# Kernel optimization log

Measured on AMD Instinct MI355X. Metric: run time of the kernel, lower is better.

The kernel has to match this reference:

```python
import jax, jax.numpy as jnp
import numpy as np

NUM_HEADS = 16
DIM_MODEL = 1024
DIM_K = DIM_MODEL // NUM_HEADS
B, S = 2, 2048


def _linear_params(key, d_in, d_out):
    kw, kb = jax.random.split(key)
    bound = 1.0 / np.sqrt(d_in)
    W = jax.random.uniform(kw, (d_out, d_in), jnp.float32, -bound, bound)
    b = jax.random.uniform(kb, (d_out,), jnp.float32, -bound, bound)
    return W, b


def setup_inputs() -> dict:
    key = jax.random.key(0)
    ks = jax.random.split(key, 7)
    Q_in = jax.random.normal(ks[0], (B, S, DIM_MODEL), jnp.float32)
    K_in = jax.random.normal(ks[1], (B, S, DIM_MODEL), jnp.float32)
    V_in = jax.random.normal(ks[2], (B, S, DIM_MODEL), jnp.float32)
    Wq, bq = _linear_params(ks[3], DIM_MODEL, DIM_MODEL)
    Wk, bk = _linear_params(ks[4], DIM_MODEL, DIM_MODEL)
    Wv, bv = _linear_params(ks[5], DIM_MODEL, DIM_MODEL)
    Wo, bo = _linear_params(ks[6], DIM_MODEL, DIM_MODEL)
    return {"Q_in": Q_in, "K_in": K_in, "V_in": V_in,
            "Wq": Wq, "bq": bq, "Wk": Wk, "bk": bk,
            "Wv": Wv, "bv": bv, "Wo": Wo, "bo": bo}


def reference(Q_in, K_in, V_in, Wq, bq, Wk, bk, Wv, bv, Wo, bo):
    # QKV projections (nn.Linear: x @ W.T + b)
    Q = Q_in @ Wq.T + bq
    K = K_in @ Wk.T + bk
    V = V_in @ Wv.T + bv
    # [B, S, D] -> [B, H, S, dk]
    def split_heads(x):
        return x.reshape(B, S, NUM_HEADS, DIM_K).transpose(0, 2, 1, 3)
    Qh, Kh, Vh = split_heads(Q), split_heads(K), split_heads(V)
    # Scaled dot-product attention
    scale = 1.0 / np.sqrt(DIM_K)
    scores = jnp.einsum('bhqd,bhkd->bhqk', Qh, Kh) * scale  # [B,H,S,S]
    attn = jax.nn.softmax(scores, axis=-1)
    out = jnp.einsum('bhqk,bhkd->bhqd', attn, Vh)  # [B,H,S,dk]
    # Merge heads -> [B, S, D]
    out = out.transpose(0, 2, 1, 3).reshape(B, S, DIM_MODEL)
    return out @ Wo.T + bo
```

## Files before the change

### kernel.cpp

```cpp
#include <hip/hip_runtime.h>
#include <stdint.h>

#define BB 2
#define SS 2048
#define DD 1024
#define HH 16
#define DKK 64
#define MT (BB*SS)

#define GSTRIDE 40

#define QSCALE 0.18033688011112042f

using short8  = __attribute__((ext_vector_type(8))) short;
using floatx4 = __attribute__((ext_vector_type(4))) float;
using u16x4   = __attribute__((ext_vector_type(4))) unsigned short;
typedef unsigned short u16;

__device__ __forceinline__ float ex2(float x) { return __builtin_amdgcn_exp2f(x); }

__device__ __forceinline__ u16 f2b(float f) {
  union { float f; unsigned u; } v; v.f = f;
  return (u16)((v.u + 0x7FFFu + ((v.u >> 16) & 1u)) >> 16);
}
__device__ __forceinline__ unsigned cvt_pk_bf16(float lo, float hi) {
  unsigned r;
  asm("v_cvt_pk_bf16_f32 %0, %1, %2" : "=v"(r) : "v"(lo), "v"(hi));
  return r;
}
__device__ __forceinline__ void pack16(const float4* p, short8& lo, short8& hi) {
  float4 x0 = p[0], x1 = p[1], x2 = p[2], x3 = p[3];
  lo[0]=(short)f2b(x0.x); lo[1]=(short)f2b(x0.y); lo[2]=(short)f2b(x0.z); lo[3]=(short)f2b(x0.w);
  lo[4]=(short)f2b(x1.x); lo[5]=(short)f2b(x1.y); lo[6]=(short)f2b(x1.z); lo[7]=(short)f2b(x1.w);
  hi[0]=(short)f2b(x2.x); hi[1]=(short)f2b(x2.y); hi[2]=(short)f2b(x2.z); hi[3]=(short)f2b(x2.w);
  hi[4]=(short)f2b(x3.x); hi[5]=(short)f2b(x3.y); hi[6]=(short)f2b(x3.z); hi[7]=(short)f2b(x3.w);
}
__device__ __forceinline__ void gload16(const u16* g, u16* l) {
  __builtin_amdgcn_global_load_lds(
      (const __attribute__((address_space(1))) void*)g,
      (__attribute__((address_space(3))) void*)l, 16, 0, 0);
}

__global__ __launch_bounds__(256) void cast_all(
    const float* __restrict__ Qin, const float* __restrict__ Kin,
    const float* __restrict__ Vin, const float* __restrict__ Wq,
    const float* __restrict__ Wk,  const float* __restrict__ Wv,
    const float* __restrict__ Wo,
    u16* __restrict__ cQ, u16* __restrict__ cK, u16* __restrict__ cV,
    u16* __restrict__ cWq, u16* __restrict__ cWk, u16* __restrict__ cWv,
    u16* __restrict__ cWo)
{
  const int y = blockIdx.y;
  if (y >= 3 && blockIdx.x >= (DD*DD/8/256)) return;
  const float* s; u16* d;
  switch (y) {
    case 0: s = Qin; d = cQ;  break;
    case 1: s = Kin; d = cK;  break;
    case 2: s = Vin; d = cV;  break;
    case 3: s = Wq;  d = cWq; break;
    case 4: s = Wk;  d = cWk; break;
    case 5: s = Wv;  d = cWv; break;
    default: s = Wo; d = cWo; break;
  }
  const size_t g = (size_t)blockIdx.x * 256 + threadIdx.x;
  float4 x0 = ((const float4*)s)[g*2], x1 = ((const float4*)s)[g*2+1];
  short8 lo;
  lo[0]=(short)f2b(x0.x); lo[1]=(short)f2b(x0.y); lo[2]=(short)f2b(x0.z); lo[3]=(short)f2b(x0.w);
  lo[4]=(short)f2b(x1.x); lo[5]=(short)f2b(x1.y); lo[6]=(short)f2b(x1.z); lo[7]=(short)f2b(x1.w);
  ((short8*)d)[g] = lo;
}
__global__ __launch_bounds__(256) void cast_w3(
    const float* __restrict__ w0, const float* __restrict__ w1,
    const float* __restrict__ w2, u16* __restrict__ o)
{
  const float* s = (blockIdx.y == 0) ? w0 : (blockIdx.y == 1) ? w1 : w2;
  u16* d = o + (size_t)blockIdx.y * (DD * DD);
  const size_t g = (size_t)blockIdx.x * 256 + threadIdx.x;
  float4 x0 = ((const float4*)s)[g*2], x1 = ((const float4*)s)[g*2+1];
  short8 lo;
  lo[0]=(short)f2b(x0.x); lo[1]=(short)f2b(x0.y); lo[2]=(short)f2b(x0.z); lo[3]=(short)f2b(x0.w);
  lo[4]=(short)f2b(x1.x); lo[5]=(short)f2b(x1.y); lo[6]=(short)f2b(x1.z); lo[7]=(short)f2b(x1.w);
  ((short8*)d)[g] = lo;
}

template<bool OUT_F32>
__device__ __forceinline__ void gemm_async(
    const u16* __restrict__ A, const u16* __restrict__ W,
    const float* __restrict__ bias, void* __restrict__ Cv,
    const int K, const int N, const int m0, const int n0, const float scale)
{
  __shared__ __align__(16) u16 sA[128*64];
  __shared__ __align__(16) u16 sB[128*64];

  const int tid  = threadIdx.x;
  const int wave = tid >> 6;
  const int lane = tid & 63;
  const int quad = lane >> 4;
  const int lr   = lane & 15;
  const int wm   = wave >> 1;
  const int wn   = wave & 1;
  const int srow = lane >> 3;
  const int swz  = (((lane & 7) ^ ((srow & 1) << 2)) << 3);

  floatx4 acc[4][4];
#pragma unroll
  for (int i = 0; i < 4; ++i)
#pragma unroll
    for (int j = 0; j < 4; ++j) acc[i][j] = (floatx4){0.f, 0.f, 0.f, 0.f};

  const u16* pA[4]; const u16* pW[4];
#pragma unroll
  for (int c = 0; c < 4; ++c) {
    const int row = (wave + c*4) * 8 + srow;
    pA[c] = A + (size_t)(m0 + row) * K + swz;
    pW[c] = W + (size_t)(n0 + row) * K + swz;
  }

  const int nk = K >> 6;
  for (int kt = 0; kt < nk; ++kt) {
    const int k0 = kt << 6;
#pragma unroll
    for (int c = 0; c < 4; ++c) {
      gload16(pA[c] + k0, sA + (wave + c*4) * 512);
      gload16(pW[c] + k0, sB + (wave + c*4) * 512);
    }
    __syncthreads();

#pragma unroll
    for (int h2 = 0; h2 < 2; ++h2) {
      const int csel = (quad << 3) + ((h2 ^ (lr & 1)) << 5);
      short8 af[4], bf[4];
#pragma unroll
      for (int t = 0; t < 4; ++t) {
        af[t] = *(const short8*)(sA + (wm*64 + t*16 + lr)*64 + csel);
        bf[t] = *(const short8*)(sB + (wn*64 + t*16 + lr)*64 + csel);
      }
#pragma unroll
      for (int i = 0; i < 4; ++i)
#pragma unroll
        for (int j = 0; j < 4; ++j)
          acc[i][j] = __builtin_amdgcn_mfma_f32_16x16x32_bf16(af[i], bf[j], acc[i][j], 0, 0, 0);
    }
    __syncthreads();
  }

#pragma unroll
  for (int i = 0; i < 4; ++i) {
    const int mb = m0 + wm*64 + i*16 + quad*4;
#pragma unroll
    for (int j = 0; j < 4; ++j) {
      const int n = n0 + wn*64 + j*16 + lr;
      const float bsv = bias[n];
#pragma unroll
      for (int r = 0; r < 4; ++r) {
        const size_t idx = (size_t)(mb + r) * N + n;
        const float v = (acc[i][j][r] + bsv) * scale;
        if (OUT_F32) ((float*)Cv)[idx] = v;
        else         ((u16*)Cv)[idx]   = f2b(v);
      }
    }
  }
}

__global__ __launch_bounds__(256, 3) void gemm_qkv_async(
    const u16* __restrict__ cQ, const u16* __restrict__ cK, const u16* __restrict__ cV,
    const u16* __restrict__ cWq, const u16* __restrict__ cWk, const u16* __restrict__ cWv,
    const float* __restrict__ bq, const float* __restrict__ bk, const float* __restrict__ bv,
    u16* __restrict__ oQ, u16* __restrict__ oK, u16* __restrict__ oV)
{
  const int bid = blockIdx.x;
  const int xcd = bid & 7;
  const int j   = bid >> 3;
  const int mat = j >> 5;
  const int r   = j & 31;
  const int m0  = ((xcd << 2) + (r >> 3)) * 128;
  const int n0  = (r & 7) * 128;
  const u16* A; const u16* W; const float* bias; u16* C;
  if (mat == 0)      { A = cQ; W = cWq; bias = bq; C = oQ; }
  else if (mat == 1) { A = cK; W = cWk; bias = bk; C = oK; }
  else               { A = cV; W = cWv; bias = bv; C = oV; }
  const float scale = (mat == 0) ? QSCALE : 1.0f;
  gemm_async<false>(A, W, bias, C, DD, DD, m0, n0, scale);
}

__global__ __launch_bounds__(256, 3) void gemm_out_async(
    const u16* __restrict__ A, const u16* __restrict__ cWo,
    const float* __restrict__ bias, float* __restrict__ C)
{
  const int bid = blockIdx.x;
  const int xcd = bid & 7;
  const int j   = bid >> 3;
  const int m0  = ((xcd << 2) + (j >> 3)) * 128;
  const int n0  = (j & 7) * 128;
  gemm_async<true>(A, cWo, bias, C, DD, DD, m0, n0, 1.0f);
}

template<bool A_BF16, bool W_BF16, bool OUT_F32>
__device__ __forceinline__ void gemm_core(
    const void* __restrict__ A, const void* __restrict__ W,
    const float* __restrict__ bias, void* __restrict__ Cv,
    const int K, const int N, const int m0, const int n0, const float scale)
{
  __shared__ __align__(16) u16 sA[128*GSTRIDE];
  __shared__ __align__(16) u16 sB[128*GSTRIDE];

  const int tid  = threadIdx.x;
  const int wave = tid >> 6;
  const int lane = tid & 63;
  const int quad = lane >> 4;
  const int lr   = lane & 15;
  const int wm   = wave >> 1;
  const int wn   = wave & 1;
  const int srow = tid >> 1;
  const int scol = (tid & 1) * 16;

  floatx4 acc[4][4];
#pragma unroll
  for (int i = 0; i < 4; ++i)
#pragma unroll
    for (int j = 0; j < 4; ++j) acc[i][j] = (floatx4){0.f, 0.f, 0.f, 0.f};

  const size_t offA = (size_t)(m0 + srow) * K + scol;
  const size_t offW = (size_t)(n0 + srow) * K + scol;

  const int nk = K >> 5;
  for (int kt = 0; kt < nk; ++kt) {
    const int k0 = kt << 5;
    short8 a0, a1, b0, b1;
    if (A_BF16) {
      const u16* p = (const u16*)A + offA + k0;
      a0 = *(const short8*)p; a1 = *(const short8*)(p + 8);
    } else {
      pack16((const float4*)((const float*)A + offA + k0), a0, a1);
    }
    if (W_BF16) {
      const u16* p = (const u16*)W + offW + k0;
      b0 = *(const short8*)p; b1 = *(const short8*)(p + 8);
    } else {
      pack16((const float4*)((const float*)W + offW + k0), b0, b1);
    }
    __syncthreads();
    *(short8*)(sA + srow * GSTRIDE + scol)     = a0;
    *(short8*)(sA + srow * GSTRIDE + scol + 8) = a1;
    *(short8*)(sB + srow * GSTRIDE + scol)     = b0;
    *(short8*)(sB + srow * GSTRIDE + scol + 8) = b1;
    __syncthreads();

    short8 af[4], bf[4];
#pragma unroll
    for (int t = 0; t < 4; ++t) {
      af[t] = *(const short8*)(sA + (wm*64 + t*16 + lr)*GSTRIDE + quad*8);
      bf[t] = *(const short8*)(sB + (wn*64 + t*16 + lr)*GSTRIDE + quad*8);
    }
#pragma unroll
    for (int i = 0; i < 4; ++i)
#pragma unroll
      for (int j = 0; j < 4; ++j)
        acc[i][j] = __builtin_amdgcn_mfma_f32_16x16x32_bf16(af[i], bf[j], acc[i][j], 0, 0, 0);
  }

#pragma unroll
  for (int i = 0; i < 4; ++i) {
    const int mb = m0 + wm*64 + i*16 + quad*4;
#pragma unroll
    for (int j = 0; j < 4; ++j) {
      const int n = n0 + wn*64 + j*16 + lr;
      const float bsv = bias[n];
#pragma unroll
      for (int r = 0; r < 4; ++r) {
        const size_t idx = (size_t)(mb + r) * N + n;
        const float v = (acc[i][j][r] + bsv) * scale;
        if (OUT_F32) ((float*)Cv)[idx] = v;
        else         ((u16*)Cv)[idx]   = f2b(v);
      }
    }
  }
}

__global__ __launch_bounds__(256, 2) void gemm_qkv_fb(
    const float* __restrict__ Qin, const float* __restrict__ Kin, const float* __restrict__ Vin,
    const u16* __restrict__ cWq, const u16* __restrict__ cWk, const u16* __restrict__ cWv,
    const float* __restrict__ bq, const float* __restrict__ bk, const float* __restrict__ bv,
    u16* __restrict__ oQ, u16* __restrict__ oK, u16* __restrict__ oV)
{
  const int wsel = blockIdx.x >> 3;
  const int n0 = (blockIdx.x & 7) * 128;
  const int m0 = blockIdx.y * 128;
  const float* A; const u16* W; const float* bias; u16* C;
  if (wsel == 0)      { A = Qin; W = cWq; bias = bq; C = oQ; }
  else if (wsel == 1) { A = Kin; W = cWk; bias = bk; C = oK; }
  else                { A = Vin; W = cWv; bias = bv; C = oV; }
  const float scale = (wsel == 0) ? QSCALE : 1.0f;
  gemm_core<false, true, false>(A, W, bias, C, DD, DD, m0, n0, scale);
}
__global__ __launch_bounds__(256, 2) void gemm_out_fb(
    const u16* __restrict__ A, const float* __restrict__ W,
    const float* __restrict__ bias, float* __restrict__ C)
{
  gemm_core<true, false, true>((const void*)A, (const void*)W, bias, C, DD, DD,
                               blockIdx.y * 128, blockIdx.x * 128, 1.0f);
}

__global__ __launch_bounds__(256) void transpose_v(
    const u16* __restrict__ Vp, u16* __restrict__ Vt)
{
  __shared__ u16 t[64 * 65];
  const int st = blockIdx.x, h = blockIdx.y, b = blockIdx.z;

  const int r  = threadIdx.x >> 2;
  const int c0 = (threadIdx.x & 3) * 16;
  const u16* src = Vp + ((size_t)(b * SS + st * 64 + r)) * DD + h * 64 + c0;
  short8 v0 = *(const short8*)src;
  short8 v1 = *(const short8*)(src + 8);
#pragma unroll
  for (int i = 0; i < 8; ++i) {
    t[r * 65 + c0 + i]     = (u16)v0[i];
    t[r * 65 + c0 + 8 + i] = (u16)v1[i];
  }
  __syncthreads();
  union { u16 a[16]; short8 v[2]; } ob;
#pragma unroll
  for (int i = 0; i < 16; ++i) ob.a[i] = t[(c0 + i) * 65 + r];
  u16* dst = Vt + (((size_t)(b * HH + h)) * DKK + r) * SS + st * 64 + c0;
  *(short8*)dst       = ob.v[0];
  *(short8*)(dst + 8) = ob.v[1];
}

__device__ __forceinline__ int aswz(int row, int cb) {
  return (row << 7) + (cb ^ ((row & 7) << 4));
}

__global__ __launch_bounds__(256, 2) void attn(
    const u16* __restrict__ Qp, const u16* __restrict__ Kp,
    const u16* __restrict__ Vt, u16* __restrict__ O)
{
  __shared__ __align__(16) char sK[2][64 * 128];
  __shared__ __align__(16) char sV[2][64 * 128];
  __shared__ __align__(16) char sP[4][32 * 128];

  const int tid = threadIdx.x, wave = tid >> 6, lane = tid & 63;
  const int quad = lane >> 4, lr = lane & 15;

  const int flat = (blockIdx.z * 16 + blockIdx.y) * 16 + blockIdx.x;
  const int swzb = (flat & 7) * 64 + (flat >> 3);
  const int qb = swzb & 15;
  const int h  = (swzb >> 4) & 15;
  const int b  = swzb >> 8;
  const size_t vbase = ((size_t)(b * HH + h)) * DKK * SS;

  short8 qf[2][2];
#pragma unroll
  for (int g = 0; g < 2; ++g) {
    const u16* qr = Qp + ((size_t)(b * SS + qb * 128 + wave * 32 + g * 16 + lr)) * DD + h * 64 + quad * 8;
    qf[g][0] = *(const short8*)qr;
    qf[g][1] = *(const short8*)(qr + 32);
  }

  floatx4 accO[2][4];
  float m_l[2] = { -3e38f, -3e38f }, l_l[2] = { 0.f, 0.f };
#pragma unroll
  for (int g = 0; g < 2; ++g)
#pragma unroll
    for (int t = 0; t < 4; ++t) accO[g][t] = (floatx4){0.f, 0.f, 0.f, 0.f};

  const int sr = tid >> 2;
  const int ce = (tid & 3) * 16;
  const u16* kp = Kp + ((size_t)(b * SS + sr)) * DD + h * 64 + ce;
  const u16* vp = Vt + vbase + (size_t)sr * SS + ce;
  const int dk0 = aswz(sr, ce * 2), dk1 = aswz(sr, ce * 2 + 16);

  short8 rk0 = *(const short8*)kp,        rk1 = *(const short8*)(kp + 8);
  short8 rv0 = *(const short8*)vp,        rv1 = *(const short8*)(vp + 8);
  *(short8*)(sK[0] + dk0) = rk0;  *(short8*)(sK[0] + dk1) = rk1;
  *(short8*)(sV[0] + dk0) = rv0;  *(short8*)(sV[0] + dk1) = rv1;
  kp += (size_t)64 * DD; vp += 64;
  rk0 = *(const short8*)kp;  rk1 = *(const short8*)(kp + 8);
  rv0 = *(const short8*)vp;  rv1 = *(const short8*)(vp + 8);
  __syncthreads();

  const int nt = SS / 64;
  for (int kt = 0; kt < nt; ++kt) {
    const int cur = kt & 1;
    if (kt < nt - 1) {
      *(short8*)(sK[cur ^ 1] + dk0) = rk0;  *(short8*)(sK[cur ^ 1] + dk1) = rk1;
      *(short8*)(sV[cur ^ 1] + dk0) = rv0;  *(short8*)(sV[cur ^ 1] + dk1) = rv1;
    }
    if (kt < nt - 2) {
      kp += (size_t)64 * DD; vp += 64;
      rk0 = *(const short8*)kp;  rk1 = *(const short8*)(kp + 8);
      rv0 = *(const short8*)vp;  rv1 = *(const short8*)(vp + 8);
    }
    const char* sKc = sK[cur];
    const char* sVc = sV[cur];
    char* sPw = sP[wave];

    short8 kf[4][2], vf[4][2];
#pragma unroll
    for (int t = 0; t < 4; ++t) {
      const int row = t * 16 + lr;
      kf[t][0] = *(const short8*)(sKc + aswz(row, quad * 16));
      kf[t][1] = *(const short8*)(sKc + aswz(row, 64 + quad * 16));
      vf[t][0] = *(const short8*)(sVc + aswz(row, quad * 16));
      vf[t][1] = *(const short8*)(sVc + aswz(row, 64 + quad * 16));
    }

    floatx4 st[2][4];
    __builtin_amdgcn_s_setprio(1);
#pragma unroll
    for (int g = 0; g < 2; ++g)
#pragma unroll
      for (int t = 0; t < 4; ++t) {
        floatx4 cc = (floatx4){0.f, 0.f, 0.f, 0.f};
        cc = __builtin_amdgcn_mfma_f32_16x16x32_bf16(kf[t][0], qf[g][0], cc, 0, 0, 0);
        cc = __builtin_amdgcn_mfma_f32_16x16x32_bf16(kf[t][1], qf[g][1], cc, 0, 0, 0);
        st[g][t] = cc;
      }
    __builtin_amdgcn_s_setprio(0);

#pragma unroll
    for (int g = 0; g < 2; ++g) {
      float mx = st[g][0][0];
#pragma unroll
      for (int t = 0; t < 4; ++t)
#pragma unroll
        for (int r = 0; r < 4; ++r) mx = fmaxf(mx, st[g][t][r]);
      mx = fmaxf(mx, __shfl_xor(mx, 16, 64));
      mx = fmaxf(mx, __shfl_xor(mx, 32, 64));

      if (!__all(mx - m_l[g] <= 11.54f)) {
        const float mn2 = fmaxf(m_l[g], mx);
        const float al = ex2(m_l[g] - mn2);
        m_l[g] = mn2;
        l_l[g] *= al;
        float arow[4];
#pragma unroll
        for (int r = 0; r < 4; ++r) arow[r] = __shfl(al, quad * 4 + r, 64);
#pragma unroll
        for (int t = 0; t < 4; ++t) {
          floatx4 o = accO[g][t];
          o[0] *= arow[0]; o[1] *= arow[1]; o[2] *= arow[2]; o[3] *= arow[3];
          accO[g][t] = o;
        }
      }
      const float mn = m_l[g];

      float rs = 0.f;
      u16x4 pk[4];
#pragma unroll
      for (int t = 0; t < 4; ++t) {
        const float p0 = ex2(st[g][t][0] - mn);
        const float p1 = ex2(st[g][t][1] - mn);
        const float p2 = ex2(st[g][t][2] - mn);
        const float p3 = ex2(st[g][t][3] - mn);
        rs += (p0 + p1) + (p2 + p3);
        union { unsigned u[2]; u16x4 v; } pp;
        pp.u[0] = cvt_pk_bf16(p0, p1);
        pp.u[1] = cvt_pk_bf16(p2, p3);
        pk[t] = pp.v;
      }
      l_l[g] += rs;

#pragma unroll
      for (int t = 0; t < 4; ++t)
        *(u16x4*)(sPw + aswz(g * 16 + lr, t * 32 + quad * 8)) = pk[t];

      short8 p0 = *(const short8*)(sPw + aswz(g * 16 + lr, quad * 16));
      short8 p1 = *(const short8*)(sPw + aswz(g * 16 + lr, 64 + quad * 16));
      __builtin_amdgcn_s_setprio(1);
#pragma unroll
      for (int t = 0; t < 4; ++t) {
        accO[g][t] = __builtin_amdgcn_mfma_f32_16x16x32_bf16(p0, vf[t][0], accO[g][t], 0, 0, 0);
        accO[g][t] = __builtin_amdgcn_mfma_f32_16x16x32_bf16(p1, vf[t][1], accO[g][t], 0, 0, 0);
      }
      __builtin_amdgcn_s_setprio(0);
    }

    __syncthreads();
  }

#pragma unroll
  for (int g = 0; g < 2; ++g) {
    l_l[g] += __shfl_xor(l_l[g], 16, 64);
    l_l[g] += __shfl_xor(l_l[g], 32, 64);
    float lrow[4];
#pragma unroll
    for (int r = 0; r < 4; ++r) lrow[r] = __shfl(l_l[g], quad * 4 + r, 64);
#pragma unroll
    for (int t = 0; t < 4; ++t)
#pragma unroll
      for (int r = 0; r < 4; ++r) {
        const int s = qb * 128 + wave * 32 + g * 16 + quad * 4 + r;
        const int d = h * 64 + t * 16 + lr;
        O[((size_t)(b * SS + s)) * DD + d] = f2b(accO[g][t][r] / lrow[r]);
      }
  }
}

extern "C" void kernel_launch(void* const* d_in, const int* in_sizes, int n_in,
                              void* d_out, int out_size, void* d_ws, size_t ws_size,
                              hipStream_t stream)
{
  const float* Qin = (const float*)d_in[0];
  const float* Kin = (const float*)d_in[1];
  const float* Vin = (const float*)d_in[2];
  const float* Wq  = (const float*)d_in[3];
  const float* bq  = (const float*)d_in[4];
  const float* Wk  = (const float*)d_in[5];
  const float* bk  = (const float*)d_in[6];
  const float* Wv  = (const float*)d_in[7];
  const float* bv  = (const float*)d_in[8];
  const float* Wo  = (const float*)d_in[9];
  const float* bo  = (const float*)d_in[10];
  float* out = (float*)d_out;

  const size_t TSZ = (size_t)MT * DD;
  const size_t WSZ = (size_t)DD * DD;
  dim3 blk(256);

  u16* cWq = (u16*)d_out;
  u16* cWk = cWq + WSZ;
  u16* cWv = cWk + WSZ;

  u16* pQ   = (u16*)d_ws;
  u16* pK   = pQ  + TSZ;
  u16* pV   = pK  + TSZ;
  u16* wsVt = pV  + TSZ;
  u16* wsO  = wsVt + TSZ;

  if (ws_size >= (8*TSZ + WSZ) * sizeof(u16)) {
    u16* cQ  = wsO + TSZ;
    u16* cK  = cQ  + TSZ;
    u16* cV  = cK  + TSZ;
    u16* cWo = cV  + TSZ;
    cast_all<<<dim3(TSZ/8/256, 7), blk, 0, stream>>>(
        Qin, Kin, Vin, Wq, Wk, Wv, Wo, cQ, cK, cV, cWq, cWk, cWv, cWo);
    gemm_qkv_async<<<dim3(768), blk, 0, stream>>>(
        cQ, cK, cV, cWq, cWk, cWv, bq, bk, bv, pQ, pK, pV);
    transpose_v<<<dim3(SS/64, HH, BB), blk, 0, stream>>>(pV, wsVt);
    attn<<<dim3(SS/128, HH, BB), blk, 0, stream>>>(pQ, pK, wsVt, wsO);
    gemm_out_async<<<dim3(256), blk, 0, stream>>>(wsO, cWo, bo, out);
  } else {
    cast_w3<<<dim3(WSZ/8/256, 3), blk, 0, stream>>>(Wq, Wk, Wv, cWq);
    gemm_qkv_fb<<<dim3(24, MT/128), blk, 0, stream>>>(
        Qin, Kin, Vin, cWq, cWk, cWv, bq, bk, bv, pQ, pK, pV);
    transpose_v<<<dim3(SS/64, HH, BB), blk, 0, stream>>>(pV, wsVt);
    attn<<<dim3(SS/128, HH, BB), blk, 0, stream>>>(pQ, pK, wsVt, wsO);
    gemm_out_fb<<<dim3(DD/128, MT/128), blk, 0, stream>>>(wsO, Wo, bo, out);
  }
}
```

Measured before the change: 231.2 us.

## Split output projection GEMM along K into two partials plus bias-add kernel

The output projection GEMM is split into two halves along the K dimension, launching 512 blocks instead of 256 so more of the GPU's compute units are occupied. Each half writes an fp32 partial result, one into the output and one into a reused workspace buffer. A separate kernel then adds the two partials and the bias. This trades extra fp32 global memory traffic and one more kernel launch for better occupancy on the small output GEMM.

```diff
diff --git a/kernel.cpp b/kernel.cpp
--- a/kernel.cpp
+++ b/kernel.cpp
@@ -87,7 +87,8 @@
 __device__ __forceinline__ void gemm_async(
     const u16* __restrict__ A, const u16* __restrict__ W,
     const float* __restrict__ bias, void* __restrict__ Cv,
-    const int K, const int N, const int m0, const int n0, const float scale)
+    const int K, const int Kext, const int N,
+    const int m0, const int n0, const float scale)
 {
   __shared__ __align__(16) u16 sA[128*64];
   __shared__ __align__(16) u16 sB[128*64];
@@ -116,7 +117,7 @@
     pW[c] = W + (size_t)(n0 + row) * K + swz;
   }
 
-  const int nk = K >> 6;
+  const int nk = Kext >> 6;
   for (int kt = 0; kt < nk; ++kt) {
     const int k0 = kt << 6;
 #pragma unroll
@@ -150,7 +151,7 @@
 #pragma unroll
     for (int j = 0; j < 4; ++j) {
       const int n = n0 + wn*64 + j*16 + lr;
-      const float bsv = bias[n];
+      const float bsv = bias ? bias[n] : 0.f;
 #pragma unroll
       for (int r = 0; r < 4; ++r) {
         const size_t idx = (size_t)(mb + r) * N + n;
@@ -180,19 +181,34 @@
   else if (mat == 1) { A = cK; W = cWk; bias = bk; C = oK; }
   else               { A = cV; W = cWv; bias = bv; C = oV; }
   const float scale = (mat == 0) ? QSCALE : 1.0f;
-  gemm_async<false>(A, W, bias, C, DD, DD, m0, n0, scale);
-}
-
-__global__ __launch_bounds__(256, 3) void gemm_out_async(
+  gemm_async<false>(A, W, bias, C, DD, DD, DD, m0, n0, scale);
+}
+
+__global__ __launch_bounds__(256, 3) void gemm_out_split(
     const u16* __restrict__ A, const u16* __restrict__ cWo,
-    const float* __restrict__ bias, float* __restrict__ C)
-{
-  const int bid = blockIdx.x;
-  const int xcd = bid & 7;
-  const int j   = bid >> 3;
-  const int m0  = ((xcd << 2) + (j >> 3)) * 128;
-  const int n0  = (j & 7) * 128;
-  gemm_async<true>(A, cWo, bias, C, DD, DD, m0, n0, 1.0f);
+    float* __restrict__ P0, float* __restrict__ P1)
+{
+  const int ksel = blockIdx.x >> 8;
+  const int sub  = blockIdx.x & 255;
+  const int xcd  = sub & 7;
+  const int j    = sub >> 3;
+  const int m0   = ((xcd << 2) + (j >> 3)) * 128;
+  const int n0   = (j & 7) * 128;
+  const int koff = ksel * 512;
+  gemm_async<true>(A + koff, cWo + koff, nullptr, ksel ? P1 : P0,
+                   DD, 512, DD, m0, n0, 1.0f);
+}
+
+__global__ __launch_bounds__(256) void add_bias(
+    float* __restrict__ out, const float* __restrict__ p1,
+    const float* __restrict__ bias)
+{
+  const size_t i = ((size_t)blockIdx.x * 256 + threadIdx.x) * 4;
+  float4 a = *(float4*)(out + i);
+  float4 b = *(const float4*)(p1 + i);
+  float4 c = *(const float4*)(bias + (i & (DD - 1)));
+  a.x += b.x + c.x; a.y += b.y + c.y; a.z += b.z + c.z; a.w += b.w + c.w;
+  *(float4*)(out + i) = a;
 }
 
 template<bool A_BF16, bool W_BF16, bool OUT_F32>
@@ -538,7 +554,9 @@
         cQ, cK, cV, cWq, cWk, cWv, bq, bk, bv, pQ, pK, pV);
     transpose_v<<<dim3(SS/64, HH, BB), blk, 0, stream>>>(pV, wsVt);
     attn<<<dim3(SS/128, HH, BB), blk, 0, stream>>>(pQ, pK, wsVt, wsO);
-    gemm_out_async<<<dim3(256), blk, 0, stream>>>(wsO, cWo, bo, out);
+    float* P1 = (float*)cQ;
+    gemm_out_split<<<dim3(512), blk, 0, stream>>>(wsO, cWo, out, P1);
+    add_bias<<<dim3((unsigned)(TSZ/4/256)), blk, 0, stream>>>(out, P1, bo);
   } else {
     cast_w3<<<dim3(WSZ/8/256, 3), blk, 0, stream>>>(Wq, Wk, Wv, cWq);
     gemm_qkv_fb<<<dim3(24, MT/128), blk, 0, stream>>>(
```

Result: no change. 234.2 us (+1.3%).
